# Kernel optimization log

Hardware: AMD Instinct MI355X
Metric: run time of the kernel (lower is better)

The kernel has to match this reference:

```python
import jax, jax.numpy as jnp
import numpy as np

NUM_HEADS = 4
HEAD_DIM = 64
BN_EPS = 1e-5


def setup_inputs() -> dict:
    key = jax.random.key(0)
    ks = jax.random.split(key, 6)
    B, C, H, W = 8, 256, 48, 48
    HD = NUM_HEADS * HEAD_DIM  # 256
    x = jax.random.normal(ks[0], (B, C, H, W), dtype=jnp.float32)
    q_w = jax.random.normal(ks[1], (HD, C), dtype=jnp.float32) * (1.0 / np.sqrt(C))
    k_w = jax.random.normal(ks[2], (HEAD_DIM, C), dtype=jnp.float32) * (1.0 / np.sqrt(C))
    v_w = jax.random.normal(ks[3], (HEAD_DIM, C), dtype=jnp.float32) * (1.0 / np.sqrt(C))
    proj_w = jax.random.normal(ks[4], (C, HD), dtype=jnp.float32) * (1.0 / np.sqrt(HD))
    proj_b = jnp.zeros((C,), dtype=jnp.float32)
    gamma = jnp.ones((C,), dtype=jnp.float32)
    beta = jnp.zeros((C,), dtype=jnp.float32)
    return {"x": x, "q_w": q_w, "k_w": k_w, "v_w": v_w,
            "proj_w": proj_w, "proj_b": proj_b, "gamma": gamma, "beta": beta}


def reference(x, q_w, k_w, v_w, proj_w, proj_b, gamma, beta):
    B, C, H, W = x.shape
    N = H * W
    scale = HEAD_DIM ** -0.5
    xf = x.reshape(B, C, N)  # 1x1 conv == channel matmul
    q = jnp.einsum('oc,bcn->bon', q_w, xf).reshape(B, NUM_HEADS, HEAD_DIM, N)
    k = jnp.einsum('dc,bcn->bdn', k_w, xf)  # shared single KV head (MQA)
    v = jnp.einsum('dc,bcn->bdn', v_w, xf)
    # scores: [B, heads, N, N]
    attn = jnp.einsum('bhdn,bdm->bhnm', q, k) * scale
    attn = jax.nn.softmax(attn, axis=-1)
    out = jnp.einsum('bhnm,bdm->bhdn', attn, v)  # [B, heads, d, N]
    out = out.reshape(B, NUM_HEADS * HEAD_DIM, N)
    out = jnp.einsum('co,bon->bcn', proj_w, out) + proj_b[None, :, None]
    out = out.reshape(B, C, H, W)
    # BatchNorm2d (training-mode batch statistics, biased variance)
    mean = jnp.mean(out, axis=(0, 2, 3), keepdims=True)
    var = jnp.var(out, axis=(0, 2, 3), keepdims=True)
    out = gamma[None, :, None, None] * (out - mean) * jax.lax.rsqrt(var + BN_EPS) + beta[None, :, None, None]
    return out + x
```

## Files before the change

### kernel.cpp

```cpp
#include <hip/hip_runtime.h>
#include <hip/hip_bf16.h>
#include <math.h>

#define BB 8
#define CCH 256
#define NN 2304
#define NH 4
#define HDIM 64
#define QKV_ROWS 384
#define BN_EPS 1e-5f
#define NTILES 36
#define HTILES 18
#define NPART 288
#define SLOG2E 0.18033688011112042f

typedef short bf16x8 __attribute__((ext_vector_type(8)));
typedef short bf16x4 __attribute__((ext_vector_type(4)));
typedef float f32x4 __attribute__((ext_vector_type(4)));

#if __has_builtin(__builtin_amdgcn_exp2f)
#define EXP2(x) __builtin_amdgcn_exp2f(x)
#else
#define EXP2(x) __expf((x) * 0.6931471805599453f)
#endif

#define MFMA32(a, b, c) __builtin_amdgcn_mfma_f32_16x16x32_bf16(a, b, c, 0, 0, 0)

__device__ __forceinline__ unsigned bfpair(float a, float b) {
    __hip_bfloat162 h = __float22bfloat162_rn(make_float2(a, b));
    return *(unsigned*)&h;
}
__device__ __forceinline__ unsigned short f2bf(float f) {
    unsigned u = __float_as_uint(f);
    u = (u + 0x7FFFu + ((u >> 16) & 1u)) >> 16;
    return (unsigned short)u;
}
__device__ __forceinline__ float bf2f(unsigned short s) {
    return __uint_as_float((unsigned)s << 16);
}

__global__ __launch_bounds__(256) void prep_k(
    const float* __restrict__ x,
    const float* __restrict__ qw, const float* __restrict__ kw,
    const float* __restrict__ vw, const float* __restrict__ pw,
    unsigned short* __restrict__ xT, unsigned short* __restrict__ xb,
    unsigned short* __restrict__ Wb, unsigned short* __restrict__ Pb)
{
    const int bid = blockIdx.x;
    const int tid = threadIdx.x;
    if (bid < 1152) {
        __shared__ float sX[64][65];
        const int b  = bid / 144;
        const int rem = bid - b * 144;
        const int nb = (rem >> 2) * 64;
        const int cb = (rem & 3) * 64;

        #pragma unroll
        for (int u = 0; u < 4; ++u) {
            int c  = (tid >> 4) + 16 * u;
            int n4 = (tid & 15) * 4;
            float4 v = *(const float4*)(x + ((size_t)(b * CCH + cb + c)) * NN + nb + n4);
            sX[c][n4+0] = v.x; sX[c][n4+1] = v.y; sX[c][n4+2] = v.z; sX[c][n4+3] = v.w;
        }
        __syncthreads();

        const int n  = tid >> 2;
        const int cg = (tid & 3) * 16;
        unsigned vals[8];
        #pragma unroll
        for (int p = 0; p < 8; ++p)
            vals[p] = bfpair(sX[cg + 2*p][n], sX[cg + 2*p + 1][n]);
        unsigned short* dst = xT + ((size_t)(b * NN + nb + n)) * CCH + cb + cg;
        *(uint4*)dst = make_uint4(vals[0], vals[1], vals[2], vals[3]);
        *(uint4*)(dst + 8) = make_uint4(vals[4], vals[5], vals[6], vals[7]);

        #pragma unroll
        for (int it = 0; it < 2; ++it) {
            int flat = tid + 256 * it;
            int row = flat >> 3;
            int n8  = (flat & 7) * 8;
            unsigned vv[4];
            #pragma unroll
            for (int p = 0; p < 4; ++p)
                vv[p] = bfpair(sX[row][n8 + 2*p], sX[row][n8 + 2*p + 1]);
            *(uint4*)(xb + ((size_t)(b * CCH + cb + row)) * NN + nb + n8) =
                make_uint4(vv[0], vv[1], vv[2], vv[3]);
        }
    } else {
        int idx = (bid - 1152) * 256 + tid;
        if (idx < 98304) {
            int o = idx >> 8, c = idx & 255;
            float v;
            if (o < 256)      v = qw[(size_t)o * CCH + c] * SLOG2E;
            else if (o < 320) v = kw[(size_t)(o - 256) * CCH + c];
            else              v = vw[(size_t)(o - 320) * CCH + c];
            Wb[idx] = f2bf(v);
        } else {
            int j = idx - 98304;
            if (j < 65536) Pb[j] = f2bf(pw[j]);
        }
    }
}

__global__ __launch_bounds__(128) void qkv_mfma_k(
    const unsigned short* __restrict__ Wb, const unsigned short* __restrict__ xT,
    unsigned short* __restrict__ Qt, unsigned short* __restrict__ Kt,
    unsigned short* __restrict__ Vn)
{
    __shared__ unsigned short sE[2][64 * 72];
    const int tid = threadIdx.x;
    const int wave = tid >> 6;
    const int lane = tid & 63;
    const int quad = lane >> 4;
    const int l15  = lane & 15;
    const int b  = blockIdx.x;
    const int nb = blockIdx.y * 64;
    const int mb = blockIdx.z * 128 + wave * 64;

    const unsigned short* Ab = Wb + (size_t)(mb + l15) * CCH + quad * 8;
    const unsigned short* Bb = xT + ((size_t)(b * NN + nb + l15)) * CCH + quad * 8;

    f32x4 C[4][4] = {};
    bf16x8 aA[2][4], bB[2][4];
    #pragma unroll
    for (int i = 0; i < 4; ++i) aA[0][i] = *(const bf16x8*)(Ab + (size_t)(16*i) * CCH);
    #pragma unroll
    for (int j = 0; j < 4; ++j) bB[0][j] = *(const bf16x8*)(Bb + (size_t)(16*j) * CCH);

    #pragma unroll
    for (int kk = 0; kk < 8; ++kk) {
        const int cur = kk & 1;
        if (kk < 7) {
            const int k1 = (kk + 1) * 32;
            #pragma unroll
            for (int i = 0; i < 4; ++i) aA[cur^1][i] = *(const bf16x8*)(Ab + (size_t)(16*i) * CCH + k1);
            #pragma unroll
            for (int j = 0; j < 4; ++j) bB[cur^1][j] = *(const bf16x8*)(Bb + (size_t)(16*j) * CCH + k1);
        }
        #pragma unroll
        for (int i = 0; i < 4; ++i)
            #pragma unroll
            for (int j = 0; j < 4; ++j)
                C[i][j] = MFMA32(aA[cur][i], bB[cur][j], C[i][j]);
    }

    unsigned short* sEw = &sE[wave][0];
    if (mb < 320) {
        #pragma unroll
        for (int i = 0; i < 4; ++i)
            #pragma unroll
            for (int j = 0; j < 4; ++j) {
                unsigned p01 = bfpair(C[i][j][0], C[i][j][1]);
                unsigned p23 = bfpair(C[i][j][2], C[i][j][3]);
                unsigned short* p = sEw + (16*j + l15) * 72 + 16*i + quad*4;
                *(unsigned*)p = p01;
                *(unsigned*)(p + 2) = p23;
            }
        if (mb < 256) {
            #pragma unroll
            for (int it = 0; it < 8; ++it) {
                int flat = lane + 64 * it;
                int row = flat >> 3;
                int o8  = (flat & 7) * 8;
                uint4 v = *(const uint4*)(sEw + row * 72 + o8);
                *(uint4*)(Qt + ((size_t)(b * NN + nb + row)) * CCH + mb + o8) = v;
            }
        } else {
            #pragma unroll
            for (int it = 0; it < 8; ++it) {
                int flat = lane + 64 * it;
                int row = flat >> 3;
                int o8  = (flat & 7) * 8;
                uint4 v = *(const uint4*)(sEw + row * 72 + o8);
                *(uint4*)(Kt + ((size_t)(b * NN + nb + row)) * 64 + o8) = v;
            }
        }
    } else {
        #pragma unroll
        for (int i = 0; i < 4; ++i)
            #pragma unroll
            for (int j = 0; j < 4; ++j) {
                unsigned p01 = bfpair(C[i][j][0], C[i][j][1]);
                unsigned p23 = bfpair(C[i][j][2], C[i][j][3]);
                unsigned short* p = sEw + (16*i + quad*4) * 72 + 16*j + l15;
                p[0]   = (unsigned short)p01;
                p[72]  = (unsigned short)(p01 >> 16);
                p[144] = (unsigned short)p23;
                p[216] = (unsigned short)(p23 >> 16);
            }
        #pragma unroll
        for (int it = 0; it < 8; ++it) {
            int flat = lane + 64 * it;
            int row = flat >> 3;
            int n8  = (flat & 7) * 8;
            uint4 v = *(const uint4*)(sEw + row * 72 + n8);
            *(uint4*)(Vn + ((size_t)(b * 64 + (mb - 320) + row)) * NN + nb + n8) = v;
        }
    }
}

__global__ __launch_bounds__(512, 4) void attn_k(
    const unsigned short* __restrict__ Qt,
    const unsigned short* __restrict__ Kt,
    const unsigned short* __restrict__ Vn,
    unsigned short* __restrict__ Ao)
{
    __shared__ __align__(16) unsigned short sKV[2 * 4 * 64 * 64];

    const int tid   = threadIdx.x;
    const int wave  = tid >> 6;
    const int lane  = tid & 63;
    const int quad  = lane >> 4;
    const int l15   = lane & 15;
    const int qslot = wave & 1;
    const int kh    = (wave >> 1) & 1;
    const int hloc  = wave >> 2;
    const int qoff  = qslot * 32;
    const int b     = blockIdx.x;
    const int nb    = blockIdx.y * 64;
    const int head  = blockIdx.z * 2 + hloc;

    const bf16x8 vone8 = {(short)0x3F80, (short)0x3F80, (short)0x3F80, (short)0x3F80,
                          (short)0x3F80, (short)0x3F80, (short)0x3F80, (short)0x3F80};

    bf16x8 bQ[2][2];
    const unsigned short* QtB = Qt + ((size_t)(b * NN + nb + qoff + l15)) * CCH + head * 64 + quad * 8;
    #pragma unroll
    for (int qt = 0; qt < 2; ++qt)
        #pragma unroll
        for (int s = 0; s < 2; ++s)
            bQ[qt][s] = *(const bf16x8*)(QtB + (size_t)(16*qt) * CCH + s * 32);

    const int srow = tid >> 3;
    const int swch = ((tid & 7) ^ (srow & 7)) * 8;
    const int krow = (srow & 3) | (((srow >> 3) & 3) << 2) | (((srow >> 2) & 1) << 4) | (srow & 32);
    const int kwch = ((tid & 7) ^ (krow & 7)) * 8;
    const int sgc8 = (tid & 7) * 8;

    bf16x8 pf[4];
    #pragma unroll
    for (int u = 0; u < 4; ++u) {
        const int keys0 = (u >> 1) * HTILES * 64;
        if ((u & 1) == 0)
            pf[u] = *(const bf16x8*)(Kt + ((size_t)(b * NN + keys0 + srow)) * 64 + sgc8);
        else
            pf[u] = *(const bf16x8*)(Vn + ((size_t)(b * 64 + srow)) * NN + keys0 + sgc8);
    }
    *(bf16x8*)(sKV + 0 * 4096 + krow * 64 + kwch) = pf[0];
    *(bf16x8*)(sKV + 1 * 4096 + srow * 64 + swch) = pf[1];
    *(bf16x8*)(sKV + 2 * 4096 + krow * 64 + kwch) = pf[2];
    *(bf16x8*)(sKV + 3 * 4096 + srow * 64 + swch) = pf[3];
    #pragma unroll
    for (int u = 0; u < 4; ++u) {
        const int keys0 = ((u >> 1) * HTILES + 1) * 64;
        if ((u & 1) == 0)
            pf[u] = *(const bf16x8*)(Kt + ((size_t)(b * NN + keys0 + srow)) * 64 + sgc8);
        else
            pf[u] = *(const bf16x8*)(Vn + ((size_t)(b * 64 + srow)) * NN + keys0 + sgc8);
    }

    f32x4 O[4][2] = {};
    f32x4 dacc[2] = {};

    for (int step = 0; step < HTILES; ++step) {
        const int cur = step & 1;
        __syncthreads();

        if (step + 1 < HTILES) {
            unsigned short* dstb = sKV + (cur ^ 1) * 16384;
            *(bf16x8*)(dstb + 0 * 4096 + krow * 64 + kwch) = pf[0];
            *(bf16x8*)(dstb + 1 * 4096 + srow * 64 + swch) = pf[1];
            *(bf16x8*)(dstb + 2 * 4096 + krow * 64 + kwch) = pf[2];
            *(bf16x8*)(dstb + 3 * 4096 + srow * 64 + swch) = pf[3];
        }
        if (step + 2 < HTILES) {
            #pragma unroll
            for (int u = 0; u < 4; ++u) {
                const int keys0 = ((u >> 1) * HTILES + step + 2) * 64;
                if ((u & 1) == 0)
                    pf[u] = *(const bf16x8*)(Kt + ((size_t)(b * NN + keys0 + srow)) * 64 + sgc8);
                else
                    pf[u] = *(const bf16x8*)(Vn + ((size_t)(b * 64 + srow)) * NN + keys0 + sgc8);
            }
        }

        const unsigned short* sKb = sKV + cur * 16384 + kh * 2 * 4096;
        const unsigned short* sVb = sKb + 4096;

        f32x4 C[4][2] = {};
        #pragma unroll
        for (int s = 0; s < 2; ++s)
            #pragma unroll
            for (int kt = 0; kt < 4; ++kt) {
                const int row = 16*kt + l15;
                const int chsw = ((s*4 + quad) ^ (row & 7)) * 8;
                bf16x8 aK = *(const bf16x8*)(sKb + row * 64 + chsw);
                C[kt][0] = MFMA32(aK, bQ[0][s], C[kt][0]);
                C[kt][1] = MFMA32(aK, bQ[1][s], C[kt][1]);
            }

        bf16x8 bP[2][2];
        #pragma unroll
        for (int kt2 = 0; kt2 < 2; ++kt2)
            #pragma unroll
            for (int qt = 0; qt < 2; ++qt) {
                union { unsigned u[4]; bf16x8 v; } xp;
                const f32x4 c0 = C[2*kt2][qt];
                const f32x4 c1 = C[2*kt2+1][qt];
                xp.u[0] = bfpair(EXP2(c0[0]), EXP2(c0[1]));
                xp.u[1] = bfpair(EXP2(c0[2]), EXP2(c0[3]));
                xp.u[2] = bfpair(EXP2(c1[0]), EXP2(c1[1]));
                xp.u[3] = bfpair(EXP2(c1[2]), EXP2(c1[3]));
                bP[kt2][qt] = xp.v;
            }

        #pragma unroll
        for (int kt2 = 0; kt2 < 2; ++kt2) {
            dacc[0] = MFMA32(vone8, bP[kt2][0], dacc[0]);
            dacc[1] = MFMA32(vone8, bP[kt2][1], dacc[1]);
        }

        #pragma unroll
        for (int jd = 0; jd < 4; ++jd)
            #pragma unroll
            for (int kt2 = 0; kt2 < 2; ++kt2) {
                const int row = 16*jd + l15;
                const int chsw = ((4*kt2 + quad) ^ (row & 7)) * 8;
                bf16x8 aV = *(const bf16x8*)(sVb + row * 64 + chsw);
                O[jd][0] = MFMA32(aV, bP[kt2][0], O[jd][0]);
                O[jd][1] = MFMA32(aV, bP[kt2][1], O[jd][1]);
            }
    }
    __syncthreads();

    float* sc = (float*)sKV;
    const int base = (hloc * 2 + qslot) * 2304 + lane * 36;
    if (kh == 1) {
        #pragma unroll
        for (int jd = 0; jd < 4; ++jd)
            #pragma unroll
            for (int qt = 0; qt < 2; ++qt)
                *(f32x4*)(sc + base + jd * 8 + qt * 4) = O[jd][qt];
        sc[base + 32] = dacc[0][0];
        sc[base + 33] = dacc[1][0];
    }
    __syncthreads();
    float rinv[2] = {0.f, 0.f};
    if (kh == 0) {
        #pragma unroll
        for (int jd = 0; jd < 4; ++jd)
            #pragma unroll
            for (int qt = 0; qt < 2; ++qt)
                O[jd][qt] += *(const f32x4*)(sc + base + jd * 8 + qt * 4);
        rinv[0] = 1.0f / (dacc[0][0] + sc[base + 32]);
        rinv[1] = 1.0f / (dacc[1][0] + sc[base + 33]);
    }
    __syncthreads();

    unsigned short* sT = (unsigned short*)sKV;
    if (kh == 0) {
        #pragma unroll
        for (int qt = 0; qt < 2; ++qt)
            #pragma unroll
            for (int jd = 0; jd < 4; ++jd) {
                unsigned lo = bfpair(O[jd][qt][0] * rinv[qt], O[jd][qt][1] * rinv[qt]);
                unsigned hi = bfpair(O[jd][qt][2] * rinv[qt], O[jd][qt][3] * rinv[qt]);
                *(uint2*)(sT + (hloc * 64 + qoff + 16*qt + l15) * 72 + 16*jd + quad*4) = make_uint2(lo, hi);
            }
    }
    __syncthreads();

    #pragma unroll
    for (int it = 0; it < 2; ++it) {
        int flat = tid + 512 * it;
        int hh   = flat >> 9;
        int row  = (flat >> 3) & 63;
        int c8   = (flat & 7) * 8;
        uint4 v = *(const uint4*)(sT + (hh * 64 + row) * 72 + c8);
        *(uint4*)(Ao + ((size_t)(b * NN + nb + row)) * CCH + (blockIdx.z * 2 + hh) * 64 + c8) = v;
    }
}

__global__ __launch_bounds__(128) void proj_mfma_k(
    const unsigned short* __restrict__ Pb, const unsigned short* __restrict__ Ao,
    const float* __restrict__ pb, unsigned short* __restrict__ projb,
    float* __restrict__ psum, float* __restrict__ psq)
{
    __shared__ unsigned short sE[2][64 * 72];
    const int tid = threadIdx.x;
    const int wave = tid >> 6;
    const int lane = tid & 63;
    const int quad = lane >> 4;
    const int l15  = lane & 15;
    const int b  = blockIdx.x;
    const int nb = blockIdx.y * 64;
    const int mb = blockIdx.z * 128 + wave * 64;
    const int part = b * NTILES + blockIdx.y;

    const unsigned short* Ab = Pb + (size_t)(mb + l15) * CCH + quad * 8;
    const unsigned short* Bb = Ao + ((size_t)(b * NN + nb + l15)) * CCH + quad * 8;

    f32x4 C[4][4] = {};
    bf16x8 aA[2][4], bB[2][4];
    #pragma unroll
    for (int i = 0; i < 4; ++i) aA[0][i] = *(const bf16x8*)(Ab + (size_t)(16*i) * CCH);
    #pragma unroll
    for (int j = 0; j < 4; ++j) bB[0][j] = *(const bf16x8*)(Bb + (size_t)(16*j) * CCH);

    #pragma unroll
    for (int kk = 0; kk < 8; ++kk) {
        const int cur = kk & 1;
        if (kk < 7) {
            const int k1 = (kk + 1) * 32;
            #pragma unroll
            for (int i = 0; i < 4; ++i) aA[cur^1][i] = *(const bf16x8*)(Ab + (size_t)(16*i) * CCH + k1);
            #pragma unroll
            for (int j = 0; j < 4; ++j) bB[cur^1][j] = *(const bf16x8*)(Bb + (size_t)(16*j) * CCH + k1);
        }
        #pragma unroll
        for (int i = 0; i < 4; ++i)
            #pragma unroll
            for (int j = 0; j < 4; ++j)
                C[i][j] = MFMA32(aA[cur][i], bB[cur][j], C[i][j]);
    }

    unsigned short* sEw = &sE[wave][0];
    #pragma unroll
    for (int i = 0; i < 4; ++i) {
        #pragma unroll
        for (int r = 0; r < 4; ++r) {
            const int ch = mb + 16*i + quad*4 + r;
            const float bias = pb[ch];
            float v0 = C[i][0][r] + bias, v1 = C[i][1][r] + bias;
            float v2 = C[i][2][r] + bias, v3 = C[i][3][r] + bias;
            C[i][0][r] = v0; C[i][1][r] = v1; C[i][2][r] = v2; C[i][3][r] = v3;
            float rs = (v0 + v1) + (v2 + v3);
            float rq = (v0*v0 + v1*v1) + (v2*v2 + v3*v3);
            rs += __shfl_xor(rs, 1); rq += __shfl_xor(rq, 1);
            rs += __shfl_xor(rs, 2); rq += __shfl_xor(rq, 2);
            rs += __shfl_xor(rs, 4); rq += __shfl_xor(rq, 4);
            rs += __shfl_xor(rs, 8); rq += __shfl_xor(rq, 8);
            if (l15 == 0) {
                psum[(size_t)ch * NPART + part] = rs;
                psq [(size_t)ch * NPART + part] = rq;
            }
        }
    }

    #pragma unroll
    for (int i = 0; i < 4; ++i)
        #pragma unroll
        for (int j = 0; j < 4; ++j) {
            unsigned p01 = bfpair(C[i][j][0], C[i][j][1]);
            unsigned p23 = bfpair(C[i][j][2], C[i][j][3]);
            unsigned short* p = sEw + (16*i + quad*4) * 72 + 16*j + l15;
            p[0]   = (unsigned short)p01;
            p[72]  = (unsigned short)(p01 >> 16);
            p[144] = (unsigned short)p23;
            p[216] = (unsigned short)(p23 >> 16);
        }
    #pragma unroll
    for (int it = 0; it < 8; ++it) {
        int flat = lane + 64 * it;
        int row = flat >> 3;
        int n8  = (flat & 7) * 8;
        uint4 v = *(const uint4*)(sEw + row * 72 + n8);
        *(uint4*)(projb + ((size_t)(b * CCH + mb + row)) * NN + nb + n8) = v;
    }
}

__global__ __launch_bounds__(256) void bn_apply_k(
    const unsigned short* __restrict__ projb, const unsigned short* __restrict__ xb,
    const float* __restrict__ psum, const float* __restrict__ psq,
    const float* __restrict__ gamma, const float* __restrict__ beta,
    float* __restrict__ out)
{
    const int tid = threadIdx.x;
    const int b = blockIdx.x;
    const int c = blockIdx.y;

    float s = 0.f, q = 0.f;
    for (int k = tid; k < NPART; k += 256) {
        s += psum[(size_t)c * NPART + k];
        q += psq [(size_t)c * NPART + k];
    }
    __shared__ float rs[256], rq[256];
    rs[tid] = s; rq[tid] = q;
    __syncthreads();
    for (int off = 128; off > 0; off >>= 1) {
        if (tid < off) { rs[tid] += rs[tid + off]; rq[tid] += rq[tid + off]; }
        __syncthreads();
    }
    const float inv_n = 1.0f / (float)(BB * NN);
    float mean = rs[0] * inv_n;
    float var  = rq[0] * inv_n - mean * mean;
    float scv = gamma[c] * rsqrtf(var + BN_EPS);
    float shv = beta[c] - mean * scv;

    #pragma unroll
    for (int it = 0; it < 2; ++it) {
        int chunk = tid + 256 * it;
        if (chunk < 288) {
            size_t base = ((size_t)(b * CCH + c)) * NN + chunk * 8;
            uint4 pv = *(const uint4*)(projb + base);
            uint4 xv = *(const uint4*)(xb + base);
            const unsigned short* pp = (const unsigned short*)&pv;
            const unsigned short* xx = (const unsigned short*)&xv;
            float4 r0, r1;
            r0.x = scv * bf2f(pp[0]) + shv + bf2f(xx[0]);
            r0.y = scv * bf2f(pp[1]) + shv + bf2f(xx[1]);
            r0.z = scv * bf2f(pp[2]) + shv + bf2f(xx[2]);
            r0.w = scv * bf2f(pp[3]) + shv + bf2f(xx[3]);
            r1.x = scv * bf2f(pp[4]) + shv + bf2f(xx[4]);
            r1.y = scv * bf2f(pp[5]) + shv + bf2f(xx[5]);
            r1.z = scv * bf2f(pp[6]) + shv + bf2f(xx[6]);
            r1.w = scv * bf2f(pp[7]) + shv + bf2f(xx[7]);
            *(float4*)(out + base) = r0;
            *(float4*)(out + base + 4) = r1;
        }
    }
}

extern "C" void kernel_launch(void* const* d_in, const int* in_sizes, int n_in,
                              void* d_out, int out_size, void* d_ws, size_t ws_size,
                              hipStream_t stream)
{
    const float* x     = (const float*)d_in[0];
    const float* qw    = (const float*)d_in[1];
    const float* kw    = (const float*)d_in[2];
    const float* vw    = (const float*)d_in[3];
    const float* pw    = (const float*)d_in[4];
    const float* pb    = (const float*)d_in[5];
    const float* gamma = (const float*)d_in[6];
    const float* beta  = (const float*)d_in[7];
    float* out = (float*)d_out;

    char* ws = (char*)d_ws;
    unsigned short* xT = (unsigned short*)ws;
    unsigned short* Ao = (unsigned short*)ws;
    unsigned short* Wb = (unsigned short*)(ws + 9437184);
    unsigned short* Pb = (unsigned short*)(ws + 9633792);
    unsigned short* Qt = (unsigned short*)(ws + 9764864);
    unsigned short* Kt = (unsigned short*)(ws + 19202048);
    unsigned short* Vn = (unsigned short*)(ws + 21561344);
    unsigned short* projb = (unsigned short*)(ws + 9764864);
    float* psum  = (float*)(ws + 28639232);
    float* psq   = (float*)(ws + 28934144);
    unsigned short* xb = (unsigned short*)(ws + 29229056);

    prep_k<<<1792, 256, 0, stream>>>(x, qw, kw, vw, pw, xT, xb, Wb, Pb);

    dim3 g1(BB, NN / 64, 3);
    qkv_mfma_k<<<g1, 128, 0, stream>>>(Wb, xT, Qt, Kt, Vn);

    dim3 g2(BB, NN / 64, NH / 2);
    attn_k<<<g2, 512, 0, stream>>>(Qt, Kt, Vn, Ao);

    dim3 g3(BB, NN / 64, 2);
    proj_mfma_k<<<g3, 128, 0, stream>>>(Pb, Ao, pb, projb, psum, psq);

    dim3 g4(BB, CCH);
    bn_apply_k<<<g4, 256, 0, stream>>>(projb, xb, psum, psq, gamma, beta, out);
}
```

Measured before the change: 195.4 us.

## Split attention waves across query rows instead of key halves

The attention kernel now gives each of the 4 waves per head 16 query rows and has them walk all 36 key tiles. Previously, pairs of waves split the keys into two halves and merged partial outputs and denominators through shared memory. This removes the cross-wave reduction and its extra barriers, halves the shared K/V buffer, and raises the occupancy hint to 8 blocks. The cost is a serial loop twice as long, with fewer independent MFMAs per wave per step to hide latency, and each wave reuses each loaded K/V tile for only one 16-row Q tile.

```diff
diff --git a/kernel.cpp b/kernel.cpp
--- a/kernel.cpp
+++ b/kernel.cpp
@@ -10,7 +10,6 @@
 #define QKV_ROWS 384
 #define BN_EPS 1e-5f
 #define NTILES 36
-#define HTILES 18
 #define NPART 288
 #define SLOG2E 0.18033688011112042f
 
@@ -199,23 +198,22 @@
     }
 }
 
-__global__ __launch_bounds__(512, 4) void attn_k(
+__global__ __launch_bounds__(512, 8) void attn_k(
     const unsigned short* __restrict__ Qt,
     const unsigned short* __restrict__ Kt,
     const unsigned short* __restrict__ Vn,
     unsigned short* __restrict__ Ao)
 {
-    __shared__ __align__(16) unsigned short sKV[2 * 4 * 64 * 64];
+    __shared__ __align__(16) unsigned short sKV[2 * 2 * 64 * 64];
 
     const int tid   = threadIdx.x;
     const int wave  = tid >> 6;
     const int lane  = tid & 63;
     const int quad  = lane >> 4;
     const int l15   = lane & 15;
-    const int qslot = wave & 1;
-    const int kh    = (wave >> 1) & 1;
+    const int qslot = wave & 3;
     const int hloc  = wave >> 2;
-    const int qoff  = qslot * 32;
+    const int qoff  = qslot * 16;
     const int b     = blockIdx.x;
     const int nb    = blockIdx.y * 64;
     const int head  = blockIdx.z * 2 + hloc;
@@ -223,13 +221,11 @@
     const bf16x8 vone8 = {(short)0x3F80, (short)0x3F80, (short)0x3F80, (short)0x3F80,
                           (short)0x3F80, (short)0x3F80, (short)0x3F80, (short)0x3F80};
 
-    bf16x8 bQ[2][2];
+    bf16x8 bQ[2];
     const unsigned short* QtB = Qt + ((size_t)(b * NN + nb + qoff + l15)) * CCH + head * 64 + quad * 8;
     #pragma unroll
-    for (int qt = 0; qt < 2; ++qt)
-        #pragma unroll
-        for (int s = 0; s < 2; ++s)
-            bQ[qt][s] = *(const bf16x8*)(QtB + (size_t)(16*qt) * CCH + s * 32);
+    for (int s = 0; s < 2; ++s)
+        bQ[s] = *(const bf16x8*)(QtB + s * 32);
 
     const int srow = tid >> 3;
     const int swch = ((tid & 7) ^ (srow & 7)) * 8;
@@ -237,57 +233,36 @@
     const int kwch = ((tid & 7) ^ (krow & 7)) * 8;
     const int sgc8 = (tid & 7) * 8;
 
-    bf16x8 pf[4];
-    #pragma unroll
-    for (int u = 0; u < 4; ++u) {
-        const int keys0 = (u >> 1) * HTILES * 64;
-        if ((u & 1) == 0)
-            pf[u] = *(const bf16x8*)(Kt + ((size_t)(b * NN + keys0 + srow)) * 64 + sgc8);
-        else
-            pf[u] = *(const bf16x8*)(Vn + ((size_t)(b * 64 + srow)) * NN + keys0 + sgc8);
-    }
+    bf16x8 pf[2];
+    pf[0] = *(const bf16x8*)(Kt + ((size_t)(b * NN + srow)) * 64 + sgc8);
+    pf[1] = *(const bf16x8*)(Vn + ((size_t)(b * 64 + srow)) * NN + sgc8);
     *(bf16x8*)(sKV + 0 * 4096 + krow * 64 + kwch) = pf[0];
     *(bf16x8*)(sKV + 1 * 4096 + srow * 64 + swch) = pf[1];
-    *(bf16x8*)(sKV + 2 * 4096 + krow * 64 + kwch) = pf[2];
-    *(bf16x8*)(sKV + 3 * 4096 + srow * 64 + swch) = pf[3];
-    #pragma unroll
-    for (int u = 0; u < 4; ++u) {
-        const int keys0 = ((u >> 1) * HTILES + 1) * 64;
-        if ((u & 1) == 0)
-            pf[u] = *(const bf16x8*)(Kt + ((size_t)(b * NN + keys0 + srow)) * 64 + sgc8);
-        else
-            pf[u] = *(const bf16x8*)(Vn + ((size_t)(b * 64 + srow)) * NN + keys0 + sgc8);
-    }
-
-    f32x4 O[4][2] = {};
-    f32x4 dacc[2] = {};
-
-    for (int step = 0; step < HTILES; ++step) {
+    pf[0] = *(const bf16x8*)(Kt + ((size_t)(b * NN + 64 + srow)) * 64 + sgc8);
+    pf[1] = *(const bf16x8*)(Vn + ((size_t)(b * 64 + srow)) * NN + 64 + sgc8);
+
+    f32x4 O[4] = {};
+    f32x4 dacc = {};
+
+    for (int step = 0; step < NTILES; ++step) {
         const int cur = step & 1;
         __syncthreads();
 
-        if (step + 1 < HTILES) {
-            unsigned short* dstb = sKV + (cur ^ 1) * 16384;
+        if (step + 1 < NTILES) {
+            unsigned short* dstb = sKV + (cur ^ 1) * 8192;
             *(bf16x8*)(dstb + 0 * 4096 + krow * 64 + kwch) = pf[0];
             *(bf16x8*)(dstb + 1 * 4096 + srow * 64 + swch) = pf[1];
-            *(bf16x8*)(dstb + 2 * 4096 + krow * 64 + kwch) = pf[2];
-            *(bf16x8*)(dstb + 3 * 4096 + srow * 64 + swch) = pf[3];
-        }
-        if (step + 2 < HTILES) {
-            #pragma unroll
-            for (int u = 0; u < 4; ++u) {
-                const int keys0 = ((u >> 1) * HTILES + step + 2) * 64;
-                if ((u & 1) == 0)
-                    pf[u] = *(const bf16x8*)(Kt + ((size_t)(b * NN + keys0 + srow)) * 64 + sgc8);
-                else
-                    pf[u] = *(const bf16x8*)(Vn + ((size_t)(b * 64 + srow)) * NN + keys0 + sgc8);
-            }
-        }
-
-        const unsigned short* sKb = sKV + cur * 16384 + kh * 2 * 4096;
+        }
+        if (step + 2 < NTILES) {
+            const int keys0 = (step + 2) * 64;
+            pf[0] = *(const bf16x8*)(Kt + ((size_t)(b * NN + keys0 + srow)) * 64 + sgc8);
+            pf[1] = *(const bf16x8*)(Vn + ((size_t)(b * 64 + srow)) * NN + keys0 + sgc8);
+        }
+
+        const unsigned short* sKb = sKV + cur * 8192;
         const unsigned short* sVb = sKb + 4096;
 
-        f32x4 C[4][2] = {};
+        f32x4 C[4] = {};
         #pragma unroll
         for (int s = 0; s < 2; ++s)
             #pragma unroll
@@ -295,30 +270,24 @@
                 const int row = 16*kt + l15;
                 const int chsw = ((s*4 + quad) ^ (row & 7)) * 8;
                 bf16x8 aK = *(const bf16x8*)(sKb + row * 64 + chsw);
-                C[kt][0] = MFMA32(aK, bQ[0][s], C[kt][0]);
-                C[kt][1] = MFMA32(aK, bQ[1][s], C[kt][1]);
-            }
-
-        bf16x8 bP[2][2];
-        #pragma unroll
-        for (int kt2 = 0; kt2 < 2; ++kt2)
-            #pragma unroll
-            for (int qt = 0; qt < 2; ++qt) {
-                union { unsigned u[4]; bf16x8 v; } xp;
-                const f32x4 c0 = C[2*kt2][qt];
-                const f32x4 c1 = C[2*kt2+1][qt];
-                xp.u[0] = bfpair(EXP2(c0[0]), EXP2(c0[1]));
-                xp.u[1] = bfpair(EXP2(c0[2]), EXP2(c0[3]));
-                xp.u[2] = bfpair(EXP2(c1[0]), EXP2(c1[1]));
-                xp.u[3] = bfpair(EXP2(c1[2]), EXP2(c1[3]));
-                bP[kt2][qt] = xp.v;
-            }
-
+                C[kt] = MFMA32(aK, bQ[s], C[kt]);
+            }
+
+        bf16x8 bP[2];
         #pragma unroll
         for (int kt2 = 0; kt2 < 2; ++kt2) {
-            dacc[0] = MFMA32(vone8, bP[kt2][0], dacc[0]);
-            dacc[1] = MFMA32(vone8, bP[kt2][1], dacc[1]);
-        }
+            union { unsigned u[4]; bf16x8 v; } xp;
+            const f32x4 c0 = C[2*kt2];
+            const f32x4 c1 = C[2*kt2+1];
+            xp.u[0] = bfpair(EXP2(c0[0]), EXP2(c0[1]));
+            xp.u[1] = bfpair(EXP2(c0[2]), EXP2(c0[3]));
+            xp.u[2] = bfpair(EXP2(c1[0]), EXP2(c1[1]));
+            xp.u[3] = bfpair(EXP2(c1[2]), EXP2(c1[3]));
+            bP[kt2] = xp.v;
+        }
+
+        dacc = MFMA32(vone8, bP[0], dacc);
+        dacc = MFMA32(vone8, bP[1], dacc);
 
         #pragma unroll
         for (int jd = 0; jd < 4; ++jd)
@@ -327,46 +296,18 @@
                 const int row = 16*jd + l15;
                 const int chsw = ((4*kt2 + quad) ^ (row & 7)) * 8;
                 bf16x8 aV = *(const bf16x8*)(sVb + row * 64 + chsw);
-                O[jd][0] = MFMA32(aV, bP[kt2][0], O[jd][0]);
-                O[jd][1] = MFMA32(aV, bP[kt2][1], O[jd][1]);
+                O[jd] = MFMA32(aV, bP[kt2], O[jd]);
             }
     }
     __syncthreads();
 
-    float* sc = (float*)sKV;
-    const int base = (hloc * 2 + qslot) * 2304 + lane * 36;
-    if (kh == 1) {
-        #pragma unroll
-        for (int jd = 0; jd < 4; ++jd)
-            #pragma unroll
-            for (int qt = 0; qt < 2; ++qt)
-                *(f32x4*)(sc + base + jd * 8 + qt * 4) = O[jd][qt];
-        sc[base + 32] = dacc[0][0];
-        sc[base + 33] = dacc[1][0];
-    }
-    __syncthreads();
-    float rinv[2] = {0.f, 0.f};
-    if (kh == 0) {
-        #pragma unroll
-        for (int jd = 0; jd < 4; ++jd)
-            #pragma unroll
-            for (int qt = 0; qt < 2; ++qt)
-                O[jd][qt] += *(const f32x4*)(sc + base + jd * 8 + qt * 4);
-        rinv[0] = 1.0f / (dacc[0][0] + sc[base + 32]);
-        rinv[1] = 1.0f / (dacc[1][0] + sc[base + 33]);
-    }
-    __syncthreads();
-
+    const float rinv = 1.0f / dacc[0];
     unsigned short* sT = (unsigned short*)sKV;
-    if (kh == 0) {
-        #pragma unroll
-        for (int qt = 0; qt < 2; ++qt)
-            #pragma unroll
-            for (int jd = 0; jd < 4; ++jd) {
-                unsigned lo = bfpair(O[jd][qt][0] * rinv[qt], O[jd][qt][1] * rinv[qt]);
-                unsigned hi = bfpair(O[jd][qt][2] * rinv[qt], O[jd][qt][3] * rinv[qt]);
-                *(uint2*)(sT + (hloc * 64 + qoff + 16*qt + l15) * 72 + 16*jd + quad*4) = make_uint2(lo, hi);
-            }
+    #pragma unroll
+    for (int jd = 0; jd < 4; ++jd) {
+        unsigned lo = bfpair(O[jd][0] * rinv, O[jd][1] * rinv);
+        unsigned hi = bfpair(O[jd][2] * rinv, O[jd][3] * rinv);
+        *(uint2*)(sT + (hloc * 64 + qoff + l15) * 72 + 16*jd + quad*4) = make_uint2(lo, hi);
     }
     __syncthreads();
 
```

Result: no change. 198.6 us (+1.6%).
